# Kernel optimization log

Hardware: AMD Instinct MI355X
Metric: run time of the kernel (lower is better)

## Reference

```python
import jax, jax.numpy as jnp
import numpy as np


def setup_inputs() -> dict:
    key = jax.random.key(0)
    kq, kk, kv = jax.random.split(key, 3)
    B, L, H, E = 4, 2048, 16, 64
    return {
        "queries": jax.random.normal(kq, (B, L, H, E), dtype=jnp.float32),
        "keys": jax.random.normal(kk, (B, L, H, E), dtype=jnp.float32),
        "values": jax.random.normal(kv, (B, L, H, E), dtype=jnp.float32),
    }


def reference(queries, keys, values):
    B, L, H, E = queries.shape
    S = keys.shape[1]
    scale = 1.0 / jnp.sqrt(jnp.asarray(E, queries.dtype))
    # scores: [B, H, L, S]
    scores = jnp.einsum("blhe,bshe->bhls", queries, keys)
    # causal mask: disallow s > l (upper triangle, diagonal=1)
    causal = jnp.triu(jnp.ones((L, S), dtype=bool), k=1)
    scores = jnp.where(causal[None, None], -jnp.inf, scores)
    A = jax.nn.softmax(scale * scores, axis=-1)
    V = jnp.einsum("bhls,bshd->blhd", A, values)
    return V
```

## Files before the change

kernel.cpp:

```cpp
#include <hip/hip_runtime.h>
#include <hip/hip_bf16.h>

typedef __attribute__((ext_vector_type(8))) short short8;
typedef __attribute__((ext_vector_type(4))) float f32x4;
typedef __attribute__((ext_vector_type(4))) float f4;
typedef __attribute__((ext_vector_type(2))) unsigned uint2v;

#define MFMA(a, b, c) __builtin_amdgcn_mfma_f32_16x16x32_bf16(a, b, c, 0, 0, 0)

constexpr int B_ = 4, L = 2048, H = 16, E = 64;
constexpr int QBLK = 128, KVBLK = 64, NW = 8;
constexpr int LDP = 72;
constexpr float LOG2E = 1.4426950408889634f;
constexpr float C2 = 14.426950408889634f;
constexpr size_t NELEM = (size_t)B_ * L * H * E;
constexpr size_t WS_NEEDED = NELEM * 2 * 3;
constexpr int TILE_SHORTS = KVBLK * E;

__device__ __forceinline__ unsigned short f2bf(float f) {
  union { float f; unsigned u; } x;
  x.f = f;
  unsigned r = x.u + 0x7fffu + ((x.u >> 16) & 1u);
  return (unsigned short)(r >> 16);
}

__device__ __forceinline__ float exp2_fast(float x) {
  float r;
  asm("v_exp_f32 %0, %1" : "=v"(r) : "v"(x));
  return r;
}
__device__ __forceinline__ unsigned cvt_pk_bf16(float lo, float hi) {
  unsigned r;
  asm("v_cvt_pk_bf16_f32 %0, %1, %2" : "=v"(r) : "v"(lo), "v"(hi));
  return r;
}

__device__ __forceinline__ void gload_lds16(const void* g, void* l) {
  __builtin_amdgcn_global_load_lds(
      (const __attribute__((address_space(1))) unsigned*)g,
      (__attribute__((address_space(3))) unsigned*)l, 16, 0, 0);
}

__device__ __forceinline__ void stage_tile8(const unsigned short* gtile,
                                            unsigned short* ltile,
                                            int wid, int lane) {
  const unsigned qb = (unsigned)wid * 1024u + (unsigned)lane * 16u;
  const unsigned qs = qb ^ (((qb >> 7) & 7u) << 4);
  gload_lds16((const char*)gtile + qs, (char*)ltile + qb);
}

__device__ __forceinline__ short8 lds_frag(const unsigned short* ltile, int row, int slot) {
  const unsigned byte = (unsigned)row * 128u +
                        ((((unsigned)slot) ^ ((unsigned)row & 7u)) << 4);
  return *(const short8*)((const char*)ltile + byte);
}

__device__ __forceinline__ void barrier_raw() {
  __builtin_amdgcn_sched_barrier(0);
  __builtin_amdgcn_s_barrier();
  __builtin_amdgcn_sched_barrier(0);
}

__global__ __launch_bounds__(256)
void convert_qk(const float* __restrict__ Q, const float* __restrict__ K,
                unsigned short* __restrict__ Qb, unsigned short* __restrict__ Kb) {
  const bool isq = (blockIdx.y == 0);
  const float* in = isq ? Q : K;
  unsigned short* out = isq ? Qb : Kb;
  const float scale = isq ? (0.125f * LOG2E) : 1.0f;
  const size_t t = (size_t)blockIdx.x * 256 + threadIdx.x;
  const size_t row = t >> 3;
  const int e0 = ((int)t & 7) * 8;
  const int h = (int)(row % H);
  const size_t bl = row / H;
  const int l = (int)(bl % L);
  const int b = (int)(bl / L);
  f4 a = *(const f4*)(in + t * 8);
  f4 c = *(const f4*)(in + t * 8 + 4);
  short8 o;
  o[0] = (short)f2bf(a[0] * scale); o[1] = (short)f2bf(a[1] * scale);
  o[2] = (short)f2bf(a[2] * scale); o[3] = (short)f2bf(a[3] * scale);
  o[4] = (short)f2bf(c[0] * scale); o[5] = (short)f2bf(c[1] * scale);
  o[6] = (short)f2bf(c[2] * scale); o[7] = (short)f2bf(c[3] * scale);
  *(short8*)(out + (((size_t)b * H + h) * L + l) * E + e0) = o;
}

__global__ __launch_bounds__(256)
void transpose_v(const float* __restrict__ V, unsigned short* __restrict__ Vt) {
  const int blk = blockIdx.x;
  const int st = blk % (L / KVBLK);
  const int bh = blk / (L / KVBLK);
  const int h = bh % H, b = bh / H;
  __shared__ unsigned short Ts[E][KVBLK + 8];
  const int tid = threadIdx.x;
  const int r = tid >> 3, e0 = (tid & 7) * 8;
  const float* vp = V + (((size_t)b * L + st * KVBLK) * H + h) * E;
#pragma unroll
  for (int rr = 0; rr < 2; ++rr) {
    const int row = rr * 32 + r;
    f4 a = *(const f4*)(vp + (size_t)row * (H * E) + e0);
    f4 c = *(const f4*)(vp + (size_t)row * (H * E) + e0 + 4);
#pragma unroll
    for (int j = 0; j < 4; ++j) Ts[e0 + j][row] = f2bf(a[j]);
#pragma unroll
    for (int j = 0; j < 4; ++j) Ts[e0 + 4 + j][row] = f2bf(c[j]);
  }
  __syncthreads();
  const int e = tid >> 2, k0 = (tid & 3) * 16;
  unsigned short* op = Vt + ((size_t)bh * (L / KVBLK) + st) * (E * KVBLK) + e * KVBLK + k0;
  *(short8*)op = *(const short8*)&Ts[e][k0];
  *(short8*)(op + 8) = *(const short8*)&Ts[e][k0 + 8];
}

__global__ __launch_bounds__(512, 6)
void fattn3(const unsigned short* __restrict__ Qb, const unsigned short* __restrict__ Kb,
            const unsigned short* __restrict__ Vt, float* __restrict__ O) {
  const int bh = blockIdx.x;
  const int qtile = blockIdx.y;
  const int b = bh >> 4, h = bh & 15;
  const int tid = threadIdx.x;
  const int wid = tid >> 6;
  const int lane = tid & 63;
  const int lg = lane >> 4, lm = lane & 15;
  const int qrow0 = qtile * QBLK + wid * 16;

  __shared__ __align__(16) unsigned short Ks[2][TILE_SHORTS];
  __shared__ __align__(16) unsigned short Vs[2][TILE_SHORTS];
  __shared__ __align__(16) unsigned short Pt[NW][16 * LDP];

  const unsigned short* qbase = Qb + ((size_t)bh * L + qrow0 + lm) * E + lg * 8;
  short8 qf0 = *(const short8*)qbase;
  short8 qf1 = *(const short8*)(qbase + 32);

  f32x4 o[4];
#pragma unroll
  for (int et = 0; et < 4; ++et) o[et] = (f32x4){0.f, 0.f, 0.f, 0.f};
  float lsum = 0.f;

  const unsigned short* kbase = Kb + (size_t)bh * L * E;
  const unsigned short* vbase = Vt + (size_t)bh * L * E;

  const int nkv = 2 * qtile + 2;
  const f32x4 cinit = (f32x4){-C2, -C2, -C2, -C2};

  stage_tile8(kbase, Ks[0], wid, lane);
  stage_tile8(vbase, Vs[0], wid, lane);

  for (int kt = 0; kt < nkv; ++kt) {
    const int cur = kt & 1, nxt = cur ^ 1;

    asm volatile("s_waitcnt lgkmcnt(0)" ::: "memory");
    barrier_raw();

    if (kt + 1 < nkv) {
      stage_tile8(kbase + (size_t)(kt + 1) * TILE_SHORTS, Ks[nxt], wid, lane);
      stage_tile8(vbase + (size_t)(kt + 1) * TILE_SHORTS, Vs[nxt], wid, lane);
      asm volatile("s_waitcnt vmcnt(2)" ::: "memory");
    } else {
      asm volatile("s_waitcnt vmcnt(0)" ::: "memory");
    }
    barrier_raw();

    const bool dead = (kt * KVBLK) > (qrow0 + 15);
    if (dead) continue;

    f32x4 stl[4];
#pragma unroll
    for (int ct = 0; ct < 4; ++ct) {
      short8 k0 = lds_frag(Ks[cur], ct * 16 + lm, lg);
      short8 k1 = lds_frag(Ks[cur], ct * 16 + lm, 4 + lg);
      f32x4 acc = cinit;
      acc = MFMA(k0, qf0, acc);
      acc = MFMA(k1, qf1, acc);
      stl[ct] = acc;
    }

    if (kt * KVBLK + KVBLK - 1 > qrow0) {
#pragma unroll
      for (int ct = 0; ct < 4; ++ct)
#pragma unroll
        for (int r = 0; r < 4; ++r) {
          const int key = kt * KVBLK + ct * 16 + lg * 4 + r;
          if (key > qrow0 + lm) stl[ct][r] = -1e30f;
        }
    }

#pragma unroll
    for (int ct = 0; ct < 4; ++ct)
#pragma unroll
      for (int r = 0; r < 4; ++r) {
        const float p = exp2_fast(stl[ct][r]);
        stl[ct][r] = p;
        lsum += p;
      }

#pragma unroll
    for (int ct = 0; ct < 4; ++ct) {
      uint2v w;
      w[0] = cvt_pk_bf16(stl[ct][0], stl[ct][1]);
      w[1] = cvt_pk_bf16(stl[ct][2], stl[ct][3]);
      *(uint2v*)&Pt[wid][lm * LDP + ct * 16 + lg * 4] = w;
    }
    short8 pf0 = *(const short8*)&Pt[wid][lm * LDP + 0 * 32 + lg * 8];
    short8 pf1 = *(const short8*)&Pt[wid][lm * LDP + 1 * 32 + lg * 8];

#pragma unroll
    for (int et = 0; et < 4; ++et) {
      short8 v0 = lds_frag(Vs[cur], et * 16 + lm, lg);
      short8 v1 = lds_frag(Vs[cur], et * 16 + lm, 4 + lg);
      o[et] = MFMA(pf0, v0, o[et]);
      o[et] = MFMA(pf1, v1, o[et]);
    }
  }

  lsum += __shfl_xor(lsum, 16);
  lsum += __shfl_xor(lsum, 32);
  float linv[4];
#pragma unroll
  for (int r = 0; r < 4; ++r) linv[r] = 1.f / __shfl(lsum, lg * 20 + r);
  float* op = O + (((size_t)b * L + qrow0 + lg * 4) * H + h) * E;
#pragma unroll
  for (int r = 0; r < 4; ++r)
#pragma unroll
    for (int et = 0; et < 4; ++et)
      op[(size_t)r * (H * E) + et * 16 + lm] = o[et][r] * linv[r];
}

constexpr int LDV_F = 72, LDP_F = 72;
__global__ __launch_bounds__(256, 2)
void fattn_v1(const float* __restrict__ Q, const float* __restrict__ K,
              const float* __restrict__ V, float* __restrict__ O) {
  const int qtile = blockIdx.x;
  const int bh = blockIdx.y;
  const int b = bh / H, h = bh % H;
  const int tid = threadIdx.x;
  const int wid = tid >> 6;
  const int lane = tid & 63;
  const int lg = lane >> 4, lm = lane & 15;
  __shared__ __align__(16) short Vs[E * LDV_F];
  __shared__ __align__(16) short Ps[4][16 * LDP_F];
  const int qrow0 = qtile * 64 + wid * 16;
  short8 qf[2];
  {
    const float* qp = Q + (((size_t)b * L + (qrow0 + lm)) * H + h) * E + lg * 8;
#pragma unroll
    for (int kc = 0; kc < 2; ++kc) {
      f4 a = *(const f4*)(qp + kc * 32);
      f4 c = *(const f4*)(qp + kc * 32 + 4);
      short8 r;
      r[0] = (short)f2bf(a[0] * 0.125f); r[1] = (short)f2bf(a[1] * 0.125f);
      r[2] = (short)f2bf(a[2] * 0.125f); r[3] = (short)f2bf(a[3] * 0.125f);
      r[4] = (short)f2bf(c[0] * 0.125f); r[5] = (short)f2bf(c[1] * 0.125f);
      r[6] = (short)f2bf(c[2] * 0.125f); r[7] = (short)f2bf(c[3] * 0.125f);
      qf[kc] = r;
    }
  }
  f32x4 o[4];
#pragma unroll
  for (int et = 0; et < 4; ++et) o[et] = (f32x4){0.f, 0.f, 0.f, 0.f};
  float mrow[4], lrow[4];
#pragma unroll
  for (int r = 0; r < 4; ++r) { mrow[r] = -1e30f; lrow[r] = 0.f; }
  const float* kbase = K + (((size_t)b * L) * H + h) * E;
  const float* vbase = V + (((size_t)b * L) * H + h) * E;
  const int nkv = qtile + 1;
  for (int kt = 0; kt < nkv; ++kt) {
    __syncthreads();
    {
      const int key = tid >> 2;
      const int eb = (tid & 3) * 16;
      const float* vp = vbase + (size_t)(kt * 64 + key) * (H * E) + eb;
#pragma unroll
      for (int i = 0; i < 4; ++i) {
        f4 v = *(const f4*)(vp + i * 4);
        Vs[(eb + i * 4 + 0) * LDV_F + key] = (short)f2bf(v[0]);
        Vs[(eb + i * 4 + 1) * LDV_F + key] = (short)f2bf(v[1]);
        Vs[(eb + i * 4 + 2) * LDV_F + key] = (short)f2bf(v[2]);
        Vs[(eb + i * 4 + 3) * LDV_F + key] = (short)f2bf(v[3]);
      }
    }
    f32x4 s[4];
#pragma unroll
    for (int ct = 0; ct < 4; ++ct) {
      f32x4 acc = (f32x4){0.f, 0.f, 0.f, 0.f};
      const float* kp = kbase + (size_t)(kt * 64 + ct * 16 + lm) * (H * E) + lg * 8;
#pragma unroll
      for (int kc = 0; kc < 2; ++kc) {
        f4 a = *(const f4*)(kp + kc * 32);
        f4 c = *(const f4*)(kp + kc * 32 + 4);
        short8 kf;
        kf[0] = (short)f2bf(a[0]); kf[1] = (short)f2bf(a[1]);
        kf[2] = (short)f2bf(a[2]); kf[3] = (short)f2bf(a[3]);
        kf[4] = (short)f2bf(c[0]); kf[5] = (short)f2bf(c[1]);
        kf[6] = (short)f2bf(c[2]); kf[7] = (short)f2bf(c[3]);
        acc = MFMA(qf[kc], kf, acc);
      }
      s[ct] = acc;
    }
    if (kt == nkv - 1) {
#pragma unroll
      for (int ct = 0; ct < 4; ++ct) {
        const int sg = kt * 64 + ct * 16 + lm;
#pragma unroll
        for (int r = 0; r < 4; ++r)
          if (sg > qrow0 + lg * 4 + r) s[ct][r] = -1e30f;
      }
    }
#pragma unroll
    for (int r = 0; r < 4; ++r) {
      float tm = fmaxf(fmaxf(s[0][r], s[1][r]), fmaxf(s[2][r], s[3][r]));
      tm = fmaxf(tm, __shfl_xor(tm, 1));
      tm = fmaxf(tm, __shfl_xor(tm, 2));
      tm = fmaxf(tm, __shfl_xor(tm, 4));
      tm = fmaxf(tm, __shfl_xor(tm, 8));
      const float mnew = fmaxf(mrow[r], tm);
      const float sc = __expf(mrow[r] - mnew);
      mrow[r] = mnew;
      float rs = 0.f;
#pragma unroll
      for (int ct = 0; ct < 4; ++ct) {
        const float p = __expf(s[ct][r] - mnew);
        s[ct][r] = p;
        rs += p;
      }
      rs += __shfl_xor(rs, 1);
      rs += __shfl_xor(rs, 2);
      rs += __shfl_xor(rs, 4);
      rs += __shfl_xor(rs, 8);
      lrow[r] = lrow[r] * sc + rs;
#pragma unroll
      for (int et = 0; et < 4; ++et) o[et][r] *= sc;
    }
#pragma unroll
    for (int ct = 0; ct < 4; ++ct)
#pragma unroll
      for (int r = 0; r < 4; ++r)
        Ps[wid][(lg * 4 + r) * LDP_F + ct * 16 + lm] = (short)f2bf(s[ct][r]);
    __syncthreads();
    short8 pf[2];
    pf[0] = *(const short8*)&Ps[wid][lm * LDP_F + 0 * 32 + lg * 8];
    pf[1] = *(const short8*)&Ps[wid][lm * LDP_F + 1 * 32 + lg * 8];
#pragma unroll
    for (int et = 0; et < 4; ++et)
#pragma unroll
      for (int kc = 0; kc < 2; ++kc) {
        short8 vf = *(const short8*)&Vs[(et * 16 + lm) * LDV_F + kc * 32 + lg * 8];
        o[et] = MFMA(pf[kc], vf, o[et]);
      }
  }
  float* op = O + (((size_t)b * L + qrow0) * H + h) * E;
#pragma unroll
  for (int r = 0; r < 4; ++r) {
    const float inv = 1.f / lrow[r];
#pragma unroll
    for (int et = 0; et < 4; ++et)
      op[(size_t)(lg * 4 + r) * (H * E) + et * 16 + lm] = o[et][r] * inv;
  }
}

extern "C" void kernel_launch(void* const* d_in, const int* in_sizes, int n_in,
                              void* d_out, int out_size, void* d_ws, size_t ws_size,
                              hipStream_t stream) {
  const float* Q = (const float*)d_in[0];
  const float* K = (const float*)d_in[1];
  const float* V = (const float*)d_in[2];
  float* Out = (float*)d_out;
  if (ws_size >= WS_NEEDED) {
    unsigned short* Qb = (unsigned short*)d_ws;
    unsigned short* Kb = Qb + NELEM;
    unsigned short* Vt = Kb + NELEM;
    dim3 gc((unsigned)(NELEM / (256 * 8)), 2);
    convert_qk<<<gc, 256, 0, stream>>>(Q, K, Qb, Kb);
    transpose_v<<<B_ * H * (L / KVBLK), 256, 0, stream>>>(V, Vt);
    dim3 grid(B_ * H, L / QBLK);
    fattn3<<<grid, 512, 0, stream>>>(Qb, Kb, Vt, Out);
  } else {
    dim3 grid(L / 64, B_ * H);
    fattn_v1<<<grid, 256, 0, stream>>>(Q, K, V, Out);
  }
}
```

Measured before the change: 85.08 us.

## Fuse Q conversion into attention kernel and schedule heaviest causal tiles first

Drops the separate Q-to-bf16 pass: each attention wave now loads its fp32 Q rows directly, applies the softmax scale, and converts to bf16 in registers. This removes one global write and read of Q along with its launch work, and shrinks the workspace requirement. The grid is also reordered so q-tiles are reversed, dispatching the longest causal blocks first for better load balance. The trade-off is that fp32 Q loads inside the attention kernel are strided across heads and less coalesced.

```diff
diff --git a/kernel.cpp b/kernel.cpp
--- a/kernel.cpp
+++ b/kernel.cpp
@@ -14,7 +14,7 @@
 constexpr float LOG2E = 1.4426950408889634f;
 constexpr float C2 = 14.426950408889634f;
 constexpr size_t NELEM = (size_t)B_ * L * H * E;
-constexpr size_t WS_NEEDED = NELEM * 2 * 3;
+constexpr size_t WS_NEEDED = NELEM * 2 * 2;
 constexpr int TILE_SHORTS = KVBLK * E;
 
 __device__ __forceinline__ unsigned short f2bf(float f) {
@@ -62,12 +62,7 @@
 }
 
 __global__ __launch_bounds__(256)
-void convert_qk(const float* __restrict__ Q, const float* __restrict__ K,
-                unsigned short* __restrict__ Qb, unsigned short* __restrict__ Kb) {
-  const bool isq = (blockIdx.y == 0);
-  const float* in = isq ? Q : K;
-  unsigned short* out = isq ? Qb : Kb;
-  const float scale = isq ? (0.125f * LOG2E) : 1.0f;
+void convert_k(const float* __restrict__ K, unsigned short* __restrict__ Kb) {
   const size_t t = (size_t)blockIdx.x * 256 + threadIdx.x;
   const size_t row = t >> 3;
   const int e0 = ((int)t & 7) * 8;
@@ -75,14 +70,14 @@
   const size_t bl = row / H;
   const int l = (int)(bl % L);
   const int b = (int)(bl / L);
-  f4 a = *(const f4*)(in + t * 8);
-  f4 c = *(const f4*)(in + t * 8 + 4);
+  f4 a = *(const f4*)(K + t * 8);
+  f4 c = *(const f4*)(K + t * 8 + 4);
   short8 o;
-  o[0] = (short)f2bf(a[0] * scale); o[1] = (short)f2bf(a[1] * scale);
-  o[2] = (short)f2bf(a[2] * scale); o[3] = (short)f2bf(a[3] * scale);
-  o[4] = (short)f2bf(c[0] * scale); o[5] = (short)f2bf(c[1] * scale);
-  o[6] = (short)f2bf(c[2] * scale); o[7] = (short)f2bf(c[3] * scale);
-  *(short8*)(out + (((size_t)b * H + h) * L + l) * E + e0) = o;
+  o[0] = (short)f2bf(a[0]); o[1] = (short)f2bf(a[1]);
+  o[2] = (short)f2bf(a[2]); o[3] = (short)f2bf(a[3]);
+  o[4] = (short)f2bf(c[0]); o[5] = (short)f2bf(c[1]);
+  o[6] = (short)f2bf(c[2]); o[7] = (short)f2bf(c[3]);
+  *(short8*)(Kb + (((size_t)b * H + h) * L + l) * E + e0) = o;
 }
 
 __global__ __launch_bounds__(256)
@@ -113,10 +108,10 @@
 }
 
 __global__ __launch_bounds__(512, 6)
-void fattn3(const unsigned short* __restrict__ Qb, const unsigned short* __restrict__ Kb,
+void fattn3(const float* __restrict__ Q, const unsigned short* __restrict__ Kb,
             const unsigned short* __restrict__ Vt, float* __restrict__ O) {
-  const int bh = blockIdx.x;
-  const int qtile = blockIdx.y;
+  const int qtile = (int)(gridDim.x - 1) - blockIdx.x;
+  const int bh = blockIdx.y;
   const int b = bh >> 4, h = bh & 15;
   const int tid = threadIdx.x;
   const int wid = tid >> 6;
@@ -128,17 +123,30 @@
   __shared__ __align__(16) unsigned short Vs[2][TILE_SHORTS];
   __shared__ __align__(16) unsigned short Pt[NW][16 * LDP];
 
-  const unsigned short* qbase = Qb + ((size_t)bh * L + qrow0 + lm) * E + lg * 8;
-  short8 qf0 = *(const short8*)qbase;
-  short8 qf1 = *(const short8*)(qbase + 32);
+  const unsigned short* kbase = Kb + (size_t)bh * L * E;
+  const unsigned short* vbase = Vt + (size_t)bh * L * E;
+
+  short8 qf0, qf1;
+  {
+    const float qsc = 0.125f * LOG2E;
+    const float* qp = Q + (((size_t)b * L + qrow0 + lm) * H + h) * E + lg * 8;
+    f4 a0 = *(const f4*)(qp);
+    f4 a1 = *(const f4*)(qp + 4);
+    f4 b0 = *(const f4*)(qp + 32);
+    f4 b1 = *(const f4*)(qp + 36);
+#pragma unroll
+    for (int j = 0; j < 4; ++j) {
+      qf0[j]     = (short)f2bf(a0[j] * qsc);
+      qf0[4 + j] = (short)f2bf(a1[j] * qsc);
+      qf1[j]     = (short)f2bf(b0[j] * qsc);
+      qf1[4 + j] = (short)f2bf(b1[j] * qsc);
+    }
+  }
 
   f32x4 o[4];
 #pragma unroll
   for (int et = 0; et < 4; ++et) o[et] = (f32x4){0.f, 0.f, 0.f, 0.f};
   float lsum = 0.f;
-
-  const unsigned short* kbase = Kb + (size_t)bh * L * E;
-  const unsigned short* vbase = Vt + (size_t)bh * L * E;
 
   const int nkv = 2 * qtile + 2;
   const f32x4 cinit = (f32x4){-C2, -C2, -C2, -C2};
@@ -366,14 +374,12 @@
   const float* V = (const float*)d_in[2];
   float* Out = (float*)d_out;
   if (ws_size >= WS_NEEDED) {
-    unsigned short* Qb = (unsigned short*)d_ws;
-    unsigned short* Kb = Qb + NELEM;
+    unsigned short* Kb = (unsigned short*)d_ws;
     unsigned short* Vt = Kb + NELEM;
-    dim3 gc((unsigned)(NELEM / (256 * 8)), 2);
-    convert_qk<<<gc, 256, 0, stream>>>(Q, K, Qb, Kb);
+    convert_k<<<(unsigned)(NELEM / (256 * 8)), 256, 0, stream>>>(K, Kb);
     transpose_v<<<B_ * H * (L / KVBLK), 256, 0, stream>>>(V, Vt);
-    dim3 grid(B_ * H, L / QBLK);
-    fattn3<<<grid, 512, 0, stream>>>(Qb, Kb, Vt, Out);
+    dim3 grid(L / QBLK, B_ * H);
+    fattn3<<<grid, 512, 0, stream>>>(Q, Kb, Vt, Out);
   } else {
     dim3 grid(L / 64, B_ * H);
     fattn_v1<<<grid, 256, 0, stream>>>(Q, K, V, Out);
```

New measurement: 108.4 us. 27.4% more time.
